# Performance work log

Measured on AMD Instinct MI355X. Metric: run time of the kernel, lower is better.

The kernel has to match this reference:

```python
import jax, jax.numpy as jnp
import numpy as np
import math

N0 = 50000      # nodes at level 0
E0 = 800000     # edges at level 0 (fixed edge buffer, masked when pooled)
D = 128         # hidden_dim == latent_dim
L = 2           # args.mpl_layers
NB = 2          # args.num_blocks (SAGEConvs per block)
RATIO = 0.5     # args.mpl_ratio
EPS = 1e-12


def setup_inputs() -> dict:
    key = jax.random.key(0)
    ks = jax.random.split(key, 6)
    x = jax.random.normal(ks[0], (N0, D), jnp.float32)
    edge_index = jax.random.randint(ks[1], (2, E0), 0, N0, jnp.int32)
    n_convs = (2 * L + 1) * NB  # down(4) + bottom(2) + up(4) = 10
    Wl = jax.random.normal(ks[2], (n_convs, D, D), jnp.float32) * 0.05
    bl = jax.random.normal(ks[3], (n_convs, D), jnp.float32) * 0.05
    Wr = jax.random.normal(ks[4], (n_convs, D, D), jnp.float32) * 0.05
    pool_p = jax.random.normal(ks[5], (L, D), jnp.float32)
    return {"x": x, "edge_index": edge_index, "Wl": Wl, "bl": bl, "Wr": Wr,
            "pool_p": pool_p}


def _sage(x, src, dst, valid, W_l, b_l, W_r, n):
    """PyG SAGEConv (mean aggr): lin_l(mean_{j->i} x_j) + lin_r(x_i).
    Invalid (masked) edges contribute neither to the sum nor the count."""
    msg = x[src] * valid[:, None]                       # [E, D]
    s = jax.ops.segment_sum(msg, dst, num_segments=n)   # [n, D]
    cnt = jax.ops.segment_sum(valid, dst, num_segments=n)
    mean = s / jnp.maximum(cnt, 1.0)[:, None]
    return mean @ W_l.T + b_l + x @ W_r.T


def _cal_ew(w, src, dst, valid, n):
    """WeightedEdgeConv.cal_ew (no_grad in original)."""
    deg = jax.ops.segment_sum(valid, src, num_segments=n)
    normed = w / jnp.where(deg > 0, deg, 1.0)
    w_send = normed[src] * valid
    aggr_w = jax.ops.segment_sum(w_send, dst, num_segments=n) + EPS
    ec = w_send / aggr_w[dst]
    return jax.lax.stop_gradient(ec), jax.lax.stop_gradient(aggr_w)


def _econv(x, src, dst, ec, n, aggregating=True):
    """WeightedEdgeConv.forward: gather -> scale by edge weight -> scatter-add."""
    if aggregating:
        return jax.ops.segment_sum(x[src] * ec[:, None], dst, num_segments=n)
    return jax.ops.segment_sum(x[dst] * ec[:, None], src, num_segments=n)


def reference(x, edge_index, Wl, bl, Wr, pool_p):
    src, dst = edge_index[0], edge_index[1]
    valid = jnp.ones((E0,), x.dtype)
    n = N0
    conv = 0
    down_outs, down_edges, ecs, perms, sizes = [], [], [], [], []
    w = jnp.ones((N0,), x.dtype)  # b_data.weights (ones by default)

    # ---- down path ----
    for l in range(L):
        for _ in range(NB):
            x = _sage(x, src, dst, valid, Wl[conv], bl[conv], Wr[conv], n)
            conv += 1
        down_outs.append(x)
        down_edges.append((src, dst, valid))
        sizes.append(n)
        ec, w = _cal_ew(w, src, dst, valid, n)
        ecs.append(ec)
        x = _econv(x, src, dst, ec, n, aggregating=True)
        # TopKPooling: score = x.p/||p||, keep top ceil(ratio*n), gate by tanh
        p = pool_p[l]
        score = x @ p / jnp.linalg.norm(p)
        k = int(math.ceil(RATIO * n))
        vals, perm = jax.lax.top_k(score, k)
        x = x[perm] * jnp.tanh(vals)[:, None]
        w = w[perm]
        new_id = jnp.full((n,), -1, jnp.int32).at[perm].set(
            jnp.arange(k, dtype=jnp.int32))
        src2, dst2 = new_id[src], new_id[dst]
        keep = ((src2 >= 0) & (dst2 >= 0)).astype(x.dtype)
        valid = valid * keep
        src = jnp.maximum(src2, 0)
        dst = jnp.maximum(dst2, 0)
        perms.append(perm)
        n = k

    # ---- bottom ----
    for _ in range(NB):
        x = _sage(x, src, dst, valid, Wl[conv], bl[conv], Wr[conv], n)
        conv += 1

    # ---- up path ----
    for i in range(L):
        u = L - 1 - i
        src, dst, valid = down_edges[u]
        n = sizes[u]
        # Unpool: scatter into zeros at kept-node indices
        x = jnp.zeros((n, x.shape[-1]), x.dtype).at[perms[u]].set(x)
        x = _econv(x, src, dst, ecs[u], n, aggregating=False)
        for _ in range(NB):
            x = _sage(x, src, dst, valid, Wl[conv], bl[conv], Wr[conv], n)
            conv += 1
        x = x + down_outs[u]  # skip connection
    return x
```

## Files before the change

kernel.cpp:

```cpp
#include <hip/hip_runtime.h>
#include <stdint.h>

#define DEV __device__ __forceinline__

constexpr int N0 = 50000;
constexpr int E0 = 800000;
constexpr int D  = 128;

typedef __attribute__((ext_vector_type(8))) short bf16x8;
typedef __attribute__((ext_vector_type(4))) float f32x4;

DEV float bf2f(unsigned u) { return __uint_as_float(u << 16); }
DEV unsigned short f2bf(float f) {
  unsigned u = __float_as_uint(f);
  unsigned r = u + 0x7fffu + ((u >> 16) & 1u);
  return (unsigned short)(r >> 16);
}

DEV unsigned wave_incl_scan(unsigned v, int lane) {
  #pragma unroll
  for (int off = 1; off < 64; off <<= 1) {
    unsigned u = __shfl_up(v, (unsigned)off);
    if (lane >= off) v += u;
  }
  return v;
}

__global__ void k_count(const int* __restrict__ src, const int* __restrict__ dst,
                        unsigned* cnt_src, unsigned* cnt_dst,
                        unsigned* __restrict__ rank_src, unsigned* __restrict__ rank_dst) {
  int e = blockIdx.x * blockDim.x + threadIdx.x;
  if (e < E0) {
    rank_src[e] = atomicAdd(&cnt_src[src[e]], 1u);
    rank_dst[e] = atomicAdd(&cnt_dst[dst[e]], 1u);
  }
}

__global__ void k_psum(const unsigned* __restrict__ in, int n, unsigned* __restrict__ part) {
  int t = threadIdx.x, lane = t & 63, w = t >> 6;
  int base = blockIdx.x * 1024 + t * 4;
  unsigned s = 0;
  #pragma unroll
  for (int j = 0; j < 4; ++j) { int i = base + j; if (i < n) s += in[i]; }
  #pragma unroll
  for (int off = 32; off >= 1; off >>= 1) s += __shfl_xor(s, off);
  __shared__ unsigned ws[4];
  if (lane == 0) ws[w] = s;
  __syncthreads();
  if (t == 0) part[blockIdx.x] = ws[0] + ws[1] + ws[2] + ws[3];
}

__global__ void k_scoff(const unsigned* __restrict__ part, int nch,
                        unsigned* __restrict__ off, unsigned* __restrict__ total_out) {
  if (threadIdx.x == 0) {
    unsigned run = 0;
    for (int c = 0; c < nch; ++c) { off[c] = run; run += part[c]; }
    *total_out = run;
  }
}

__global__ void k_sapply(const unsigned* __restrict__ in, const unsigned* __restrict__ choff,
                         int n, unsigned* __restrict__ out) {
  int t = threadIdx.x, lane = t & 63, w = t >> 6;
  int base = blockIdx.x * 1024 + t * 4;
  unsigned v[4]; unsigned s = 0;
  #pragma unroll
  for (int j = 0; j < 4; ++j) { int i = base + j; v[j] = (i < n) ? in[i] : 0u; s += v[j]; }
  unsigned incl = wave_incl_scan(s, lane);
  __shared__ unsigned wsum[4], woff[4];
  if (lane == 63) wsum[w] = incl;
  __syncthreads();
  if (t == 0) { unsigned run = 0; for (int j = 0; j < 4; ++j) { woff[j] = run; run += wsum[j]; } }
  __syncthreads();
  unsigned run = choff[blockIdx.x] + woff[w] + incl - s;
  #pragma unroll
  for (int j = 0; j < 4; ++j) {
    int i = base + j;
    if (i < n) out[i] = run;
    run += v[j];
  }
}

__global__ void k_fill2(const int* __restrict__ src, const int* __restrict__ dst,
                        const unsigned* __restrict__ rank_src, const unsigned* __restrict__ rank_dst,
                        const unsigned* __restrict__ indptr_src, const unsigned* __restrict__ indptr_dst,
                        int* __restrict__ adj_src, int* __restrict__ adj_dst) {
  int e = blockIdx.x * blockDim.x + threadIdx.x;
  if (e < E0) {
    int s = src[e], d = dst[e];
    adj_dst[indptr_dst[d] + rank_dst[e]] = s;
    adj_src[indptr_src[s] + rank_src[e]] = d;
  }
}

__global__ void k_adj_next2(const int* __restrict__ adjd, const int* __restrict__ adjs,
                            const int* __restrict__ new_id,
                            int* __restrict__ outd, int* __restrict__ outs) {
  int pos = blockIdx.x * blockDim.x + threadIdx.x;
  if (pos < E0) {
    int a = adjd[pos];
    outd[pos] = (a >= 0) ? new_id[a] : -1;
    int b = adjs[pos];
    outs[pos] = (b >= 0) ? new_id[b] : -1;
  }
}

__global__ void k_adj_next(const int* __restrict__ adj_prev, const int* __restrict__ new_id,
                           int* __restrict__ adj_out) {
  int pos = blockIdx.x * blockDim.x + threadIdx.x;
  if (pos < E0) {
    int a = adj_prev[pos];
    adj_out[pos] = (a >= 0) ? new_id[a] : -1;
  }
}

__global__ void k_wt(const float* __restrict__ Wl, const float* __restrict__ Wr, float* __restrict__ BT) {
  int idx = blockIdx.x * blockDim.x + threadIdx.x;
  if (idx < 4 * 256 * 128) {
    int o = idx & 127;
    int k = (idx >> 7) & 255;
    int c = idx >> 15;
    float v = (k < 128) ? Wl[(c * 128 + o) * 128 + k] : Wr[(c * 128 + o) * 128 + (k - 128)];
    BT[idx] = v;
  }
}

__global__ void k_wt_pk(const float* __restrict__ Wl, const float* __restrict__ Wr,
                        unsigned short* __restrict__ Bhi, unsigned short* __restrict__ Blo) {
  int idx = blockIdx.x * blockDim.x + threadIdx.x;
  if (idx >= 6 * 8 * 8 * 64) return;
  int l  = idx & 63;
  int ct = (idx >> 6) & 7;
  int ks = (idx >> 9) & 7;
  int c  = idx >> 12;
  int k0 = ks * 32 + (l >> 4) * 8;
  int o  = ct * 16 + (l & 15);
  int conv = c + 4;
  const float* Wrow = (k0 < 128) ? (Wl + ((size_t)conv * 128 + o) * 128 + k0)
                                 : (Wr + ((size_t)conv * 128 + o) * 128 + (k0 - 128));
  size_t base = (size_t)idx * 8;
  #pragma unroll
  for (int j = 0; j < 8; ++j) {
    float wv = Wrow[j];
    unsigned short h = f2bf(wv);
    Bhi[base + j] = h;
    Blo[base + j] = f2bf(wv - bf2f(h));
  }
}

template<bool BF, bool MASKED>
__global__ void k_sage(const void* __restrict__ xv, const int* __restrict__ adj,
                       const unsigned* __restrict__ indptr, const int* __restrict__ orig,
                       int n, float* __restrict__ mean) {
  int wid = (blockIdx.x * blockDim.x + threadIdx.x) >> 6;
  int lane = threadIdx.x & 63;
  if (wid >= n) return;
  int o = orig ? orig[wid] : wid;
  unsigned s0 = indptr[o], s1 = indptr[o + 1];
  const float* xf = (const float*)xv;
  const unsigned* xb = (const unsigned*)xv;
  float a0 = 0.f, a1 = 0.f, cnt = 0.f;
  unsigned idx = s0;
  for (; idx + 4 <= s1; idx += 4) {
    int ad[4];
    #pragma unroll
    for (int j = 0; j < 4; ++j) ad[j] = adj[idx + j];
    #pragma unroll
    for (int j = 0; j < 4; ++j) {
      if (!MASKED || ad[j] >= 0) {
        float x0, x1;
        if (BF) { unsigned u = xb[(size_t)ad[j] * 64 + lane]; x0 = bf2f(u & 0xffffu); x1 = bf2f(u >> 16); }
        else    { float2 v = *(const float2*)(xf + (size_t)ad[j] * D + lane * 2); x0 = v.x; x1 = v.y; }
        a0 += x0; a1 += x1; cnt += 1.f;
      }
    }
  }
  for (; idx < s1; ++idx) {
    int a = adj[idx];
    if (!MASKED || a >= 0) {
      float x0, x1;
      if (BF) { unsigned u = xb[(size_t)a * 64 + lane]; x0 = bf2f(u & 0xffffu); x1 = bf2f(u >> 16); }
      else    { float2 v = *(const float2*)(xf + (size_t)a * D + lane * 2); x0 = v.x; x1 = v.y; }
      a0 += x0; a1 += x1; cnt += 1.f;
    }
  }
  if (!MASKED) cnt = (float)(s1 - s0);
  float inv = 1.0f / fmaxf(cnt, 1.0f);
  *(float2*)(mean + (size_t)wid * D + lane * 2) = make_float2(a0 * inv, a1 * inv);
}

template<bool BF, bool MASKED>
__global__ void k_econv2(const void* __restrict__ xv, const int* __restrict__ adj,
                         const float* __restrict__ ecs, const unsigned* __restrict__ indptr,
                         const int* __restrict__ orig, int n,
                         float* __restrict__ out, unsigned* __restrict__ outbf) {
  int wid = (blockIdx.x * blockDim.x + threadIdx.x) >> 6;
  int lane = threadIdx.x & 63;
  if (wid >= n) return;
  int o = orig ? orig[wid] : wid;
  unsigned s0 = indptr[o], s1 = indptr[o + 1];
  const float* xf = (const float*)xv;
  const unsigned* xb = (const unsigned*)xv;
  float a0 = 0.f, a1 = 0.f;
  unsigned idx = s0;
  for (; idx + 4 <= s1; idx += 4) {
    int ad[4]; float wv[4];
    #pragma unroll
    for (int j = 0; j < 4; ++j) { ad[j] = adj[idx + j]; wv[j] = ecs[idx + j]; }
    #pragma unroll
    for (int j = 0; j < 4; ++j) {
      if (!MASKED || ad[j] >= 0) {
        float x0, x1;
        if (BF) { unsigned u = xb[(size_t)ad[j] * 64 + lane]; x0 = bf2f(u & 0xffffu); x1 = bf2f(u >> 16); }
        else    { float2 v = *(const float2*)(xf + (size_t)ad[j] * D + lane * 2); x0 = v.x; x1 = v.y; }
        a0 = fmaf(wv[j], x0, a0); a1 = fmaf(wv[j], x1, a1);
      }
    }
  }
  for (; idx < s1; ++idx) {
    int a = adj[idx]; float wgt = ecs[idx];
    if (!MASKED || a >= 0) {
      float x0, x1;
      if (BF) { unsigned u = xb[(size_t)a * 64 + lane]; x0 = bf2f(u & 0xffffu); x1 = bf2f(u >> 16); }
      else    { float2 v = *(const float2*)(xf + (size_t)a * D + lane * 2); x0 = v.x; x1 = v.y; }
      a0 = fmaf(wgt, x0, a0); a1 = fmaf(wgt, x1, a1);
    }
  }
  *(float2*)(out + (size_t)wid * D + lane * 2) = make_float2(a0, a1);
  if (outbf) {
    unsigned p = (unsigned)f2bf(a0) | ((unsigned)f2bf(a1) << 16);
    outbf[(size_t)wid * 64 + lane] = p;
  }
}

__launch_bounds__(256)
__global__ void k_conv_gemm(const float* __restrict__ mean, const float* __restrict__ xin,
                            const float* __restrict__ BT, const float* __restrict__ bias,
                            float* __restrict__ y, unsigned short* __restrict__ ybf, int n) {
  __shared__ float As[64][17];
  __shared__ float Bs[16][128];
  int tid = threadIdx.x;
  int tx = tid & 15, ty = tid >> 4;
  int row0 = blockIdx.x * 64;
  float acc[4][8];
  #pragma unroll
  for (int r = 0; r < 4; ++r)
    #pragma unroll
    for (int c = 0; c < 8; ++c) acc[r][c] = 0.f;

  int lm = tid >> 2;
  int lk = (tid & 3) * 4;
  int bk = tid >> 4;
  int bo = (tid & 15) * 8;

  for (int kc = 0; kc < 16; ++kc) {
    int k0 = kc * 16;
    const float* A = (k0 < 128) ? mean : xin;
    int kk = k0 & 127;
    int gr = row0 + lm;
    float4 av = make_float4(0.f, 0.f, 0.f, 0.f);
    if (gr < n) av = *(const float4*)(A + (size_t)gr * D + kk + lk);
    As[lm][lk + 0] = av.x; As[lm][lk + 1] = av.y; As[lm][lk + 2] = av.z; As[lm][lk + 3] = av.w;
    float4 bv0 = *(const float4*)(BT + (size_t)(k0 + bk) * 128 + bo);
    float4 bv1 = *(const float4*)(BT + (size_t)(k0 + bk) * 128 + bo + 4);
    *(float4*)&Bs[bk][bo] = bv0;
    *(float4*)&Bs[bk][bo + 4] = bv1;
    __syncthreads();
    #pragma unroll
    for (int k = 0; k < 16; ++k) {
      float a[4];
      #pragma unroll
      for (int r = 0; r < 4; ++r) a[r] = As[ty * 4 + r][k];
      float4 b0 = *(const float4*)&Bs[k][tx * 4];
      float4 b1 = *(const float4*)&Bs[k][64 + tx * 4];
      float bb[8] = {b0.x, b0.y, b0.z, b0.w, b1.x, b1.y, b1.z, b1.w};
      #pragma unroll
      for (int r = 0; r < 4; ++r)
        #pragma unroll
        for (int c = 0; c < 8; ++c)
          acc[r][c] = fmaf(a[r], bb[c], acc[r][c]);
    }
    __syncthreads();
  }
  float4 bs0 = *(const float4*)(bias + tx * 4);
  float4 bs1 = *(const float4*)(bias + 64 + tx * 4);
  #pragma unroll
  for (int r = 0; r < 4; ++r) {
    int gr = row0 + ty * 4 + r;
    if (gr < n) {
      float4 o0 = make_float4(acc[r][0] + bs0.x, acc[r][1] + bs0.y, acc[r][2] + bs0.z, acc[r][3] + bs0.w);
      float4 o1 = make_float4(acc[r][4] + bs1.x, acc[r][5] + bs1.y, acc[r][6] + bs1.z, acc[r][7] + bs1.w);
      *(float4*)(y + (size_t)gr * D + tx * 4) = o0;
      *(float4*)(y + (size_t)gr * D + 64 + tx * 4) = o1;
      if (ybf) {
        ushort4 p0; p0.x = f2bf(o0.x); p0.y = f2bf(o0.y); p0.z = f2bf(o0.z); p0.w = f2bf(o0.w);
        ushort4 p1; p1.x = f2bf(o1.x); p1.y = f2bf(o1.y); p1.z = f2bf(o1.z); p1.w = f2bf(o1.w);
        *(ushort4*)(ybf + (size_t)gr * D + tx * 4) = p0;
        *(ushort4*)(ybf + (size_t)gr * D + 64 + tx * 4) = p1;
      }
    }
  }
}

__launch_bounds__(256)
__global__ void k_gemm_mfma(const float* __restrict__ mean, const float* __restrict__ xin,
                            const unsigned short* __restrict__ Bhi, const unsigned short* __restrict__ Blo,
                            const float* __restrict__ bias, const float* __restrict__ skip,
                            float* __restrict__ y, unsigned short* __restrict__ ybf, int n) {
  int tid = threadIdx.x;
  int lane = tid & 63, w = tid >> 6;
  int row0 = blockIdx.x * 64 + w * 16;
  int arow = row0 + (lane & 15);
  int kgrp = lane >> 4;
  bool rowok = arow < n;
  f32x4 acc[8];
  #pragma unroll
  for (int ct = 0; ct < 8; ++ct) acc[ct] = f32x4{0.f, 0.f, 0.f, 0.f};

  #pragma unroll
  for (int ks = 0; ks < 8; ++ks) {
    const float* A = (ks < 4) ? mean : xin;
    int kk = (ks & 3) * 32 + kgrp * 8;
    float av[8];
    if (rowok) {
      float4 a0 = *(const float4*)(A + (size_t)arow * D + kk);
      float4 a1 = *(const float4*)(A + (size_t)arow * D + kk + 4);
      av[0] = a0.x; av[1] = a0.y; av[2] = a0.z; av[3] = a0.w;
      av[4] = a1.x; av[5] = a1.y; av[6] = a1.z; av[7] = a1.w;
    } else {
      #pragma unroll
      for (int j = 0; j < 8; ++j) av[j] = 0.f;
    }
    bf16x8 ahi, alo;
    #pragma unroll
    for (int j = 0; j < 8; ++j) {
      unsigned short h = f2bf(av[j]);
      ahi[j] = (short)h;
      alo[j] = (short)f2bf(av[j] - bf2f(h));
    }
    #pragma unroll
    for (int ct = 0; ct < 8; ++ct) {
      size_t boff = (((size_t)ks * 8 + ct) * 64 + lane) * 8;
      bf16x8 bh = *(const bf16x8*)(Bhi + boff);
      bf16x8 bl = *(const bf16x8*)(Blo + boff);
      acc[ct] = __builtin_amdgcn_mfma_f32_16x16x32_bf16(ahi, bh, acc[ct], 0, 0, 0);
      acc[ct] = __builtin_amdgcn_mfma_f32_16x16x32_bf16(alo, bh, acc[ct], 0, 0, 0);
      acc[ct] = __builtin_amdgcn_mfma_f32_16x16x32_bf16(ahi, bl, acc[ct], 0, 0, 0);
    }
  }
  int ccol = lane & 15;
  #pragma unroll
  for (int ct = 0; ct < 8; ++ct) {
    int col = ct * 16 + ccol;
    float bb = bias[col];
    #pragma unroll
    for (int r = 0; r < 4; ++r) {
      int row = row0 + kgrp * 4 + r;
      if (row < n) {
        float v = acc[ct][r] + bb;
        if (skip) v += skip[(size_t)row * D + col];
        y[(size_t)row * D + col] = v;
        if (ybf) ybf[(size_t)row * D + col] = f2bf(v);
      }
    }
  }
}

__global__ void k_deg_len(const unsigned* __restrict__ indptr, int n, float* __restrict__ deg) {
  int j = blockIdx.x * blockDim.x + threadIdx.x;
  if (j < n) deg[j] = (float)(indptr[j + 1] - indptr[j]);
}

__global__ void k_deg_mask(const int* __restrict__ adj_src, const unsigned* __restrict__ indptr_src,
                           const int* __restrict__ orig, int n, float* __restrict__ deg) {
  int j = blockIdx.x * blockDim.x + threadIdx.x;
  if (j >= n) return;
  int o = orig ? orig[j] : j;
  unsigned s0 = indptr_src[o], s1 = indptr_src[o + 1];
  float d = 0.f;
  for (unsigned i = s0; i < s1; ++i) d += (adj_src[i] >= 0) ? 1.f : 0.f;
  deg[j] = d;
}

template<bool MASKED>
__global__ void k_ew_dst(const int* __restrict__ adj, const unsigned* __restrict__ indptr,
                         const int* __restrict__ orig, const float* __restrict__ w,
                         const float* __restrict__ deg, int n,
                         float* __restrict__ ws_slot, float* __restrict__ aggrw,
                         float* __restrict__ ec_slot) {
  int j = blockIdx.x * blockDim.x + threadIdx.x;
  if (j >= n) return;
  int o = orig ? orig[j] : j;
  unsigned s0 = indptr[o], s1 = indptr[o + 1];
  float s = 1e-12f;
  for (unsigned pos = s0; pos < s1; ++pos) {
    int a = adj[pos];
    float ws = 0.f;
    if (!MASKED || a >= 0) {
      float d = deg[a];
      ws = (w ? w[a] : 1.0f) / (d > 0.f ? d : 1.0f);
    }
    ws_slot[pos] = ws;
    s += ws;
  }
  aggrw[j] = s;
  float inv = 1.0f / s;
  for (unsigned pos = s0; pos < s1; ++pos) ec_slot[pos] = ws_slot[pos] * inv;
}

template<bool MASKED>
__global__ void k_ew_src(const int* __restrict__ adj_src, const unsigned* __restrict__ indptr_src,
                         const int* __restrict__ orig, const float* __restrict__ w,
                         const float* __restrict__ deg, const float* __restrict__ aggrw, int n,
                         float* __restrict__ ec_slot) {
  int j = blockIdx.x * blockDim.x + threadIdx.x;
  if (j >= n) return;
  int o = orig ? orig[j] : j;
  unsigned s0 = indptr_src[o], s1 = indptr_src[o + 1];
  float d = deg[j];
  float wn = (w ? w[j] : 1.0f) / (d > 0.f ? d : 1.0f);
  for (unsigned pos = s0; pos < s1; ++pos) {
    int a = adj_src[pos];
    ec_slot[pos] = (!MASKED || a >= 0) ? (wn / aggrw[a]) : 0.f;
  }
}

DEV unsigned mono_key(float f) {
  unsigned u = __float_as_uint(f);
  return (u & 0x80000000u) ? ~u : (u | 0x80000000u);
}

__global__ void k_score(const float* __restrict__ x, const float* __restrict__ p,
                        int n, float* __restrict__ score, unsigned* __restrict__ keys) {
  int wid = (blockIdx.x * blockDim.x + threadIdx.x) >> 6;
  int lane = threadIdx.x & 63;
  if (wid >= n) return;
  float p0 = p[lane * 2], p1 = p[lane * 2 + 1];
  const float2 xv = *(const float2*)(x + (size_t)wid * D + lane * 2);
  float partial = xv.x * p0 + xv.y * p1;
  float pn = p0 * p0 + p1 * p1;
  #pragma unroll
  for (int off = 32; off >= 1; off >>= 1) {
    partial += __shfl_xor(partial, off);
    pn += __shfl_xor(pn, off);
  }
  if (lane == 0) {
    float sc = partial * (1.0f / sqrtf(pn));
    score[wid] = sc;
    keys[wid] = mono_key(sc);
  }
}

__launch_bounds__(1024)
__global__ void k_select(const unsigned* __restrict__ keys, int n, int k,
                         unsigned* __restrict__ state) {
  __shared__ unsigned bins[256];
  __shared__ unsigned sh_prefix, sh_r;
  int t = threadIdx.x;
  if (t == 0) { sh_prefix = 0u; sh_r = (unsigned)k; }
  for (int byte = 3; byte >= 0; --byte) {
    if (t < 256) bins[t] = 0u;
    __syncthreads();
    unsigned prefix = sh_prefix;
    unsigned mask = (byte == 3) ? 0u : (0xFFFFFFFFu << ((byte + 1) * 8));
    for (int i = t; i < n; i += 1024) {
      unsigned key = keys[i];
      if ((key & mask) == (prefix & mask))
        atomicAdd(&bins[(key >> (byte * 8)) & 255], 1u);
    }
    __syncthreads();
    if (t == 0) {
      unsigned r = sh_r; int b;
      for (b = 255; b > 0; --b) {
        unsigned c = bins[b];
        if (c >= r) break;
        r -= c;
      }
      sh_prefix = prefix | (((unsigned)b) << (byte * 8));
      sh_r = r;
    }
    __syncthreads();
  }
  if (t == 0) { state[0] = sh_prefix; state[1] = sh_r; }
}

__global__ void k_flags(const unsigned* __restrict__ keys, const unsigned* __restrict__ state,
                        int n, uint2* __restrict__ part) {
  int t = threadIdx.x, lane = t & 63, w = t >> 6;
  int base = blockIdx.x * 1024 + t * 4;
  unsigned T = state[0];
  unsigned cnt = 0;
  #pragma unroll
  for (int j = 0; j < 4; ++j) {
    int i = base + j;
    if (i < n) {
      unsigned key = keys[i];
      cnt += (key > T ? 1u : 0u) + ((key == T ? 1u : 0u) << 16);
    }
  }
  #pragma unroll
  for (int off = 32; off >= 1; off >>= 1) cnt += __shfl_xor(cnt, off);
  __shared__ unsigned ws[4];
  if (lane == 0) ws[w] = cnt;
  __syncthreads();
  if (t == 0) {
    unsigned s = ws[0] + ws[1] + ws[2] + ws[3];
    part[blockIdx.x] = make_uint2(s & 0xffffu, s >> 16);
  }
}

__global__ void k_choff(const uint2* __restrict__ part, int nch, uint2* __restrict__ off) {
  if (threadIdx.x == 0) {
    unsigned g = 0, e = 0;
    for (int c = 0; c < nch; ++c) { off[c] = make_uint2(g, e); g += part[c].x; e += part[c].y; }
  }
}

__global__ void k_pack2(const unsigned* __restrict__ keys, const unsigned* __restrict__ state,
                        const uint2* __restrict__ choff, const float* __restrict__ aggrw,
                        const int* __restrict__ orig, int n,
                        int* __restrict__ perm, int* __restrict__ new_id,
                        float* __restrict__ w_next, int* __restrict__ orig_next) {
  int t = threadIdx.x, lane = t & 63, w = t >> 6;
  int base = blockIdx.x * 1024 + t * 4;
  unsigned T = state[0], r = state[1];
  unsigned f[4];
  unsigned cnt = 0;
  #pragma unroll
  for (int j = 0; j < 4; ++j) {
    int i = base + j;
    unsigned key = (i < n) ? keys[i] : 0u;
    unsigned gt = (i < n && key > T) ? 1u : 0u;
    unsigned eq = (i < n && key == T) ? 1u : 0u;
    f[j] = gt | (eq << 1);
    cnt += gt + (eq << 16);
  }
  unsigned incl = wave_incl_scan(cnt, lane);
  __shared__ unsigned wsum[4], woff[4];
  if (lane == 63) wsum[w] = incl;
  __syncthreads();
  if (t == 0) { unsigned run = 0; for (int j = 0; j < 4; ++j) { woff[j] = run; run += wsum[j]; } }
  __syncthreads();
  unsigned before = woff[w] + incl - cnt;
  uint2 o0 = choff[blockIdx.x];
  unsigned gt_b = o0.x + (before & 0xffffu);
  unsigned eq_b = o0.y + (before >> 16);
  #pragma unroll
  for (int j = 0; j < 4; ++j) {
    int i = base + j;
    if (i >= n) break;
    unsigned gt = f[j] & 1u, eq = (f[j] >> 1) & 1u;
    bool sel = gt || (eq && eq_b < r);
    if (sel) {
      int pos = (int)(gt_b + (eq_b < r ? eq_b : r));
      perm[pos] = i;
      new_id[i] = pos;
      w_next[pos] = aggrw[i];
      orig_next[pos] = orig ? orig[i] : i;
    } else {
      new_id[i] = -1;
    }
    gt_b += gt; eq_b += eq;
  }
}

__global__ void k_gate(const float* __restrict__ xin, const int* __restrict__ perm,
                       const float* __restrict__ score, int k, float* __restrict__ xout,
                       unsigned* __restrict__ outbf) {
  int wid = (blockIdx.x * blockDim.x + threadIdx.x) >> 6;
  int lane = threadIdx.x & 63;
  if (wid >= k) return;
  int j = perm[wid];
  float g = tanhf(score[j]);
  float2 v = *(const float2*)(xin + (size_t)j * D + lane * 2);
  v.x *= g; v.y *= g;
  *(float2*)(xout + (size_t)wid * D + lane * 2) = v;
  if (outbf) {
    unsigned p = (unsigned)f2bf(v.x) | ((unsigned)f2bf(v.y) << 16);
    outbf[(size_t)wid * 64 + lane] = p;
  }
}

__global__ void k_scatter_bf(const float* __restrict__ xin, const int* __restrict__ perm,
                             int k, unsigned* __restrict__ outbf) {
  int wid = (blockIdx.x * blockDim.x + threadIdx.x) >> 6;
  int lane = threadIdx.x & 63;
  if (wid >= k) return;
  int p = perm[wid];
  float2 v = *(const float2*)(xin + (size_t)wid * D + lane * 2);
  unsigned pk = (unsigned)f2bf(v.x) | ((unsigned)f2bf(v.y) << 16);
  outbf[(size_t)p * 64 + lane] = pk;
}

extern "C" void kernel_launch(void* const* d_in, const int* in_sizes, int n_in,
                              void* d_out, int out_size, void* d_ws, size_t ws_size,
                              hipStream_t stream) {
  const float* x_in   = (const float*)d_in[0];
  const int*   ei     = (const int*)d_in[1];
  const int*   src0   = ei;
  const int*   dst0   = ei + E0;
  const float* Wl     = (const float*)d_in[2];
  const float* bl     = (const float*)d_in[3];
  const float* Wr     = (const float*)d_in[4];
  const float* pool_p = (const float*)d_in[5];
  float* out = (float*)d_out;

  const int n0 = N0, k0 = 25000, n1 = 25000, k1 = 12500, n2 = 12500;
  const int NCH0 = (N0 + 1023) / 1024;

  char* ws = (char*)d_ws;
  size_t off = 0;
  auto alloc = [&](size_t bytes) -> char* {
    char* p = ws + off;
    off += (bytes + 255) & ~(size_t)255;
    return p;
  };
  const size_t NBY = (size_t)N0 * D * 4;
  float* B0    = (float*)alloc(NBY);
  float* B1    = (float*)alloc(NBY);
  float* B2    = (float*)alloc(NBY);
  float* down0 = (float*)alloc(NBY);
  float* down1 = (float*)alloc(NBY / 2);
  unsigned* MA = (unsigned*)alloc((size_t)N0 * D * 2);
  unsigned* MB = (unsigned*)alloc((size_t)N0 * D * 2);
  int* adj0_dst = (int*)alloc(E0 * 4);
  int* adj0_src = (int*)alloc(E0 * 4);
  int* adj1_dst = (int*)alloc(E0 * 4);
  int* adj1_src = (int*)alloc(E0 * 4);
  float* ec0_src = (float*)alloc(E0 * 4);
  float* ec1_src = (float*)alloc(E0 * 4);
  float* ec_dst  = (float*)alloc(E0 * 4);
  float* ws_slot = (float*)alloc(E0 * 4);
  int* adj2_dst  = (int*)ws_slot;
  unsigned* rank_src = (unsigned*)alloc(E0 * 4);
  unsigned* rank_dst = (unsigned*)alloc(E0 * 4);
  unsigned* indptr_dst = (unsigned*)alloc((N0 + 1) * 4);
  unsigned* indptr_src = (unsigned*)alloc((N0 + 1) * 4);
  unsigned* cnt_src = (unsigned*)alloc(N0 * 4);
  unsigned* cnt_dst = (unsigned*)alloc(N0 * 4);
  float* deg   = (float*)alloc(N0 * 4);
  float* aggrw = (float*)alloc(N0 * 4);
  float* w1 = (float*)alloc(n1 * 4);
  float* w2 = (float*)alloc(n2 * 4);
  float* score = (float*)alloc(N0 * 4);
  unsigned* keys = (unsigned*)alloc(N0 * 4);
  int* perm0 = (int*)alloc(k0 * 4);
  int* perm1 = (int*)alloc(k1 * 4);
  int* orig1 = (int*)alloc(k0 * 4);
  int* orig2 = (int*)alloc(k1 * 4);
  int* new_id = (int*)alloc(N0 * 4);
  unsigned* state = (unsigned*)alloc(8);
  unsigned* spart = (unsigned*)alloc(64 * 4);
  unsigned* soff  = (unsigned*)alloc(64 * 4);
  uint2* ppart = (uint2*)alloc(64 * 8);
  uint2* poff  = (uint2*)alloc(64 * 8);
  float* BT = (float*)alloc((size_t)4 * 256 * 128 * 4);
  unsigned short* Bhi = (unsigned short*)alloc((size_t)6 * 8 * 8 * 64 * 8 * 2);
  unsigned short* Blo = (unsigned short*)alloc((size_t)6 * 8 * 8 * 64 * 8 * 2);

  const int EG = (E0 + 255) / 256;

  auto scan_np1 = [&](const unsigned* in, unsigned* outp, int n, int nch) {
    k_psum<<<nch, 256, 0, stream>>>(in, n, spart);
    k_scoff<<<1, 64, 0, stream>>>(spart, nch, soff, outp + n);
    k_sapply<<<nch, 256, 0, stream>>>(in, soff, n, outp);
  };

  hipMemsetAsync(cnt_src, 0, N0 * 4, stream);
  hipMemsetAsync(cnt_dst, 0, N0 * 4, stream);
  k_count<<<EG, 256, 0, stream>>>(src0, dst0, cnt_src, cnt_dst, rank_src, rank_dst);
  scan_np1(cnt_src, indptr_src, N0, NCH0);
  scan_np1(cnt_dst, indptr_dst, N0, NCH0);
  k_fill2<<<EG, 256, 0, stream>>>(src0, dst0, rank_src, rank_dst, indptr_src, indptr_dst,
                                  adj0_src, adj0_dst);
  k_wt<<<(4 * 256 * 128 + 255) / 256, 256, 0, stream>>>(Wl, Wr, BT);
  k_wt_pk<<<(6 * 8 * 8 * 64 + 255) / 256, 256, 0, stream>>>(Wl, Wr, Bhi, Blo);

  auto gemm = [&](const float* meanb, const float* xin, float* yout, unsigned short* ybf,
                  int n, int cidx) {
    k_conv_gemm<<<(n + 63) / 64, 256, 0, stream>>>(meanb, xin, BT + (size_t)cidx * 256 * 128,
                                                   bl + cidx * 128, yout, ybf, n);
  };
  auto gemm_mx = [&](const float* meanb, const float* xin, float* yout, unsigned short* ybf,
                     const float* skip, int n, int cidx) {
    size_t o = (size_t)(cidx - 4) * 8 * 8 * 64 * 8;
    k_gemm_mfma<<<(n + 63) / 64, 256, 0, stream>>>(meanb, xin, Bhi + o, Blo + o,
                                                   bl + cidx * 128, skip, yout, ybf, n);
  };

  auto pool_sel = [&](const float* xpool, int n, int kk, int level, const int* orig,
                      int* perm, float* w_next, int* orig_next,
                      float* xout, unsigned* xout_bf) {
    int nch = (n + 1023) / 1024;
    k_score<<<(n + 3) / 4, 256, 0, stream>>>(xpool, pool_p + level * D, n, score, keys);
    k_select<<<1, 1024, 0, stream>>>(keys, n, kk, state);
    k_flags<<<nch, 256, 0, stream>>>(keys, state, n, ppart);
    k_choff<<<1, 64, 0, stream>>>(ppart, nch, poff);
    k_pack2<<<nch, 256, 0, stream>>>(keys, state, poff, aggrw, orig, n, perm, new_id, w_next, orig_next);
    k_gate<<<(kk + 3) / 4, 256, 0, stream>>>(xpool, perm, score, kk, xout, xout_bf);
  };

  k_sage<false, false><<<(n0 + 3) / 4, 256, 0, stream>>>(x_in, adj0_dst, indptr_dst, nullptr, n0, B1);
  gemm(B1, x_in, B2, nullptr, n0, 0);
  k_sage<false, false><<<(n0 + 3) / 4, 256, 0, stream>>>(B2, adj0_dst, indptr_dst, nullptr, n0, B1);
  gemm(B1, B2, down0, nullptr, n0, 1);
  k_deg_len<<<(n0 + 255) / 256, 256, 0, stream>>>(indptr_src, n0, deg);
  k_ew_dst<false><<<(n0 + 255) / 256, 256, 0, stream>>>(adj0_dst, indptr_dst, nullptr, nullptr, deg, n0,
                                                        ws_slot, aggrw, ec_dst);
  k_ew_src<false><<<(n0 + 255) / 256, 256, 0, stream>>>(adj0_src, indptr_src, nullptr, nullptr, deg, aggrw,
                                                        n0, ec0_src);
  k_econv2<false, false><<<(n0 + 3) / 4, 256, 0, stream>>>(down0, adj0_dst, ec_dst, indptr_dst, nullptr,
                                                           n0, B1, nullptr);
  pool_sel(B1, n0, k0, 0, nullptr, perm0, w1, orig1, B2, nullptr);
  k_adj_next2<<<EG, 256, 0, stream>>>(adj0_dst, adj0_src, new_id, adj1_dst, adj1_src);

  k_sage<false, true><<<(n1 + 3) / 4, 256, 0, stream>>>(B2, adj1_dst, indptr_dst, orig1, n1, B1);
  gemm(B1, B2, B0, nullptr, n1, 2);
  k_sage<false, true><<<(n1 + 3) / 4, 256, 0, stream>>>(B0, adj1_dst, indptr_dst, orig1, n1, B1);
  gemm(B1, B0, down1, nullptr, n1, 3);
  k_deg_mask<<<(n1 + 255) / 256, 256, 0, stream>>>(adj1_src, indptr_src, orig1, n1, deg);
  k_ew_dst<true><<<(n1 + 255) / 256, 256, 0, stream>>>(adj1_dst, indptr_dst, orig1, w1, deg, n1,
                                                       ws_slot, aggrw, ec_dst);
  k_ew_src<true><<<(n1 + 255) / 256, 256, 0, stream>>>(adj1_src, indptr_src, orig1, w1, deg, aggrw,
                                                       n1, ec1_src);
  k_econv2<false, true><<<(n1 + 3) / 4, 256, 0, stream>>>(down1, adj1_dst, ec_dst, indptr_dst, orig1,
                                                          n1, B1, nullptr);
  pool_sel(B1, n1, k1, 1, orig1, perm1, w2, orig2, B2, MA);
  k_adj_next<<<EG, 256, 0, stream>>>(adj1_dst, new_id, adj2_dst);

  k_sage<true, true><<<(n2 + 3) / 4, 256, 0, stream>>>(MA, adj2_dst, indptr_dst, orig2, n2, B1);
  gemm_mx(B1, B2, B0, (unsigned short*)MB, nullptr, n2, 4);
  k_sage<true, true><<<(n2 + 3) / 4, 256, 0, stream>>>(MB, adj2_dst, indptr_dst, orig2, n2, B1);
  gemm_mx(B1, B0, B2, nullptr, nullptr, n2, 5);

  hipMemsetAsync(MA, 0, (size_t)n1 * D * 2, stream);
  k_scatter_bf<<<(n2 + 3) / 4, 256, 0, stream>>>(B2, perm1, n2, MA);
  k_econv2<true, true><<<(n1 + 3) / 4, 256, 0, stream>>>(MA, adj1_src, ec1_src, indptr_src, orig1,
                                                         n1, B1, MB);
  k_sage<true, true><<<(n1 + 3) / 4, 256, 0, stream>>>(MB, adj1_dst, indptr_dst, orig1, n1, B0);
  gemm_mx(B0, B1, B2, (unsigned short*)MA, nullptr, n1, 6);
  k_sage<true, true><<<(n1 + 3) / 4, 256, 0, stream>>>(MA, adj1_dst, indptr_dst, orig1, n1, B0);
  gemm_mx(B0, B2, B1, nullptr, down1, n1, 7);

  hipMemsetAsync(MA, 0, (size_t)n0 * D * 2, stream);
  k_scatter_bf<<<(n1 + 3) / 4, 256, 0, stream>>>(B1, perm0, n1, MA);
  k_econv2<true, false><<<(n0 + 3) / 4, 256, 0, stream>>>(MA, adj0_src, ec0_src, indptr_src, nullptr,
                                                          n0, B2, MB);
  k_sage<true, false><<<(n0 + 3) / 4, 256, 0, stream>>>(MB, adj0_dst, indptr_dst, nullptr, n0, B1);
  gemm_mx(B1, B2, B0, (unsigned short*)MA, nullptr, n0, 8);
  k_sage<true, false><<<(n0 + 3) / 4, 256, 0, stream>>>(MA, adj0_dst, indptr_dst, nullptr, n0, B1);
  gemm_mx(B1, B0, out, nullptr, down0, n0, 9);
}
```

Baseline: 1.221 ms.

## Split single-block radix select into multi-block histogram and pick kernels

Replaces the single 1024-thread radix-select kernel with a per-byte pass of a 256-block histogram kernel (shared-memory bins merged into global bins with atomics) followed by a one-thread pick kernel that updates the prefix and remainder. Each byte pass now spreads the scan over many CUs instead of one, so the serial single-block select on up to 50k keys is no longer the cost. In exchange it adds about 8 extra kernel launches per pooling level plus global atomics.

```diff
diff --git a/kernel.cpp b/kernel.cpp
--- a/kernel.cpp
+++ b/kernel.cpp
@@ -451,37 +451,43 @@
   }
 }
 
-__launch_bounds__(1024)
-__global__ void k_select(const unsigned* __restrict__ keys, int n, int k,
-                         unsigned* __restrict__ state) {
-  __shared__ unsigned bins[256];
-  __shared__ unsigned sh_prefix, sh_r;
+__global__ void k_sel_init(unsigned* bins, unsigned* state, int k) {
   int t = threadIdx.x;
-  if (t == 0) { sh_prefix = 0u; sh_r = (unsigned)k; }
-  for (int byte = 3; byte >= 0; --byte) {
-    if (t < 256) bins[t] = 0u;
-    __syncthreads();
-    unsigned prefix = sh_prefix;
-    unsigned mask = (byte == 3) ? 0u : (0xFFFFFFFFu << ((byte + 1) * 8));
-    for (int i = t; i < n; i += 1024) {
-      unsigned key = keys[i];
-      if ((key & mask) == (prefix & mask))
-        atomicAdd(&bins[(key >> (byte * 8)) & 255], 1u);
-    }
-    __syncthreads();
-    if (t == 0) {
-      unsigned r = sh_r; int b;
-      for (b = 255; b > 0; --b) {
-        unsigned c = bins[b];
-        if (c >= r) break;
-        r -= c;
-      }
-      sh_prefix = prefix | (((unsigned)b) << (byte * 8));
-      sh_r = r;
-    }
-    __syncthreads();
-  }
-  if (t == 0) { state[0] = sh_prefix; state[1] = sh_r; }
+  if (t < 256) bins[t] = 0u;
+  if (t == 0) { state[0] = 0u; state[1] = (unsigned)k; }
+}
+
+__global__ void k_hist(const unsigned* __restrict__ keys, int n, const unsigned* __restrict__ state,
+                       unsigned* __restrict__ bins, int byte) {
+  __shared__ unsigned lb[256];
+  for (int i = threadIdx.x; i < 256; i += blockDim.x) lb[i] = 0u;
+  __syncthreads();
+  unsigned prefix = state[0];
+  unsigned mask = (byte == 3) ? 0u : (0xFFFFFFFFu << ((byte + 1) * 8));
+  for (int i = blockIdx.x * blockDim.x + threadIdx.x; i < n; i += gridDim.x * blockDim.x) {
+    unsigned key = keys[i];
+    if ((key & mask) == (prefix & mask))
+      atomicAdd(&lb[(key >> (byte * 8)) & 255], 1u);
+  }
+  __syncthreads();
+  for (int i = threadIdx.x; i < 256; i += blockDim.x)
+    if (lb[i]) atomicAdd(&bins[i], lb[i]);
+}
+
+__global__ void k_pick(unsigned* bins, unsigned* state, int byte) {
+  if (threadIdx.x == 0) {
+    unsigned r = state[1];
+    int b;
+    for (b = 255; b > 0; --b) {
+      unsigned c = bins[b];
+      if (c >= r) break;
+      r -= c;
+    }
+    state[0] |= ((unsigned)b) << (byte * 8);
+    state[1] = r;
+  }
+  __syncthreads();
+  for (int i = threadIdx.x; i < 256; i += blockDim.x) bins[i] = 0u;
 }
 
 __global__ void k_flags(const unsigned* __restrict__ keys, const unsigned* __restrict__ state,
@@ -649,6 +655,7 @@
   int* orig1 = (int*)alloc(k0 * 4);
   int* orig2 = (int*)alloc(k1 * 4);
   int* new_id = (int*)alloc(N0 * 4);
+  unsigned* bins  = (unsigned*)alloc(256 * 4);
   unsigned* state = (unsigned*)alloc(8);
   unsigned* spart = (unsigned*)alloc(64 * 4);
   unsigned* soff  = (unsigned*)alloc(64 * 4);
@@ -693,7 +700,11 @@
                       float* xout, unsigned* xout_bf) {
     int nch = (n + 1023) / 1024;
     k_score<<<(n + 3) / 4, 256, 0, stream>>>(xpool, pool_p + level * D, n, score, keys);
-    k_select<<<1, 1024, 0, stream>>>(keys, n, kk, state);
+    k_sel_init<<<1, 256, 0, stream>>>(bins, state, kk);
+    for (int byte = 3; byte >= 0; --byte) {
+      k_hist<<<256, 256, 0, stream>>>(keys, n, state, bins, byte);
+      k_pick<<<1, 256, 0, stream>>>(bins, state, byte);
+    }
     k_flags<<<nch, 256, 0, stream>>>(keys, state, n, ppart);
     k_choff<<<1, 64, 0, stream>>>(ppart, nch, poff);
     k_pack2<<<nch, 256, 0, stream>>>(keys, state, poff, aggrw, orig, n, perm, new_id, w_next, orig_next);
```

Result: faster. 1.192 ms (-2.3%).
